# Kernel tuning notes

Measured on AMD Instinct MI355X. Metric: run time of the kernel, lower is better.

Reference implementation:

```python
import jax, jax.numpy as jnp
import numpy as np

DIM = 768
H = 12          # num query heads
KV = 6          # num kv heads
GS = H // KV    # group size = 2
HD = DIM // H   # head dim = 64


def setup_inputs() -> dict:
    key = jax.random.key(0)
    ks = jax.random.split(key, 6)
    B, P = 8, 1024
    s = DIM ** -0.5
    x = jax.random.normal(ks[0], (B, P, DIM), dtype=jnp.float32)
    Wq = jax.random.normal(ks[1], (DIM, DIM), dtype=jnp.float32) * s
    Wk = jax.random.normal(ks[2], (DIM, KV * HD), dtype=jnp.float32) * s
    Wv = jax.random.normal(ks[3], (DIM, KV * HD), dtype=jnp.float32) * s
    Wp = jax.random.normal(ks[4], (DIM, DIM), dtype=jnp.float32) * s
    bp = jnp.zeros((DIM,), dtype=jnp.float32)
    return {"x": x, "Wq": Wq, "Wk": Wk, "Wv": Wv, "Wp": Wp, "bp": bp}


def reference(x, Wq, Wk, Wv, Wp, bp):
    B, P, C = x.shape
    scale = HD ** -0.5
    # projections; consecutive heads i*GS..(i+1)*GS-1 form kv-group i (torch.split dim=1)
    q = (x @ Wq).reshape(B, P, KV, GS, HD).transpose(0, 2, 3, 1, 4) * scale  # [B,KV,GS,P,d]
    k = (x @ Wk).reshape(B, P, KV, HD).transpose(0, 2, 1, 3)                 # [B,KV,P,d]
    v = (x @ Wv).reshape(B, P, KV, HD).transpose(0, 2, 1, 3)                 # [B,KV,P,d]

    scores = jnp.einsum('bghqd,bgkd->bghqk', q, k)      # [B,KV,GS,P,P]
    w = jax.nn.softmax(scores, axis=-1)                  # attn_drop=0 (eval)
    att = jnp.einsum('bghqk,bgkd->bghqd', w, v)          # [B,KV,GS,P,d]

    # per-group row-matched gaussian-ish noise (torch get_gaussian), vectorized over KV groups
    y = P * HD
    flat = att.reshape(B, KV, GS, y)                     # rows = groups within kv-group
    M = jax.random.uniform(jax.random.key(42), (KV, GS, y), dtype=flat.dtype)
    di = jnp.arange(min(GS, y))
    M = M.at[:, di, di].set(0.0)                         # sparse: zero diagonal
    m_mean = M.mean(axis=-1, keepdims=True)
    m_std = jnp.std(M, axis=-1, ddof=1, keepdims=True)   # torch.std is unbiased
    m_std = jnp.where(m_std == 0, jnp.ones_like(m_std), m_std)
    Z = (M - m_mean) / m_std                             # [KV,GS,y], shared across batch
    r_mean = flat.mean(axis=-1, keepdims=True)           # [B,KV,GS,1]
    r_std = jnp.std(flat, axis=-1, ddof=1, keepdims=True)
    flat = flat - (Z[None] * r_std + r_mean)

    att = flat.reshape(B, KV, GS, P, HD).reshape(B, H, P, HD)
    out = att.transpose(0, 2, 1, 3).reshape(B, P, C) @ Wp + bp  # proj_drop=0
    return out
```

## Files before the change

kernel.cpp:

```cpp
#include <hip/hip_runtime.h>
#include <hip/hip_bf16.h>
#include <math.h>


#define NTHREADS 256

typedef __bf16 bf16x8 __attribute__((ext_vector_type(8)));
typedef float f32x4 __attribute__((ext_vector_type(4)));

#define MFMA16(a, b, c) __builtin_amdgcn_mfma_f32_16x16x32_bf16(a, b, c, 0, 0, 0)

#define QSCALE 0.18033688011112042f

__device__ __forceinline__ float fexp2(float x) {
#if __has_builtin(__builtin_amdgcn_exp2f)
    return __builtin_amdgcn_exp2f(x);
#else
    return __expf(x * 0.6931471805599453f);
#endif
}

__device__ __forceinline__ void gload16(const void* g, void* l) {
    __builtin_amdgcn_global_load_lds(
        (const __attribute__((address_space(1))) void*)g,
        (__attribute__((address_space(3))) void*)l, 16, 0, 0);
}

__device__ __forceinline__ unsigned rotl_u32(unsigned x, int r) {
    return (x << r) | (x >> (32 - r));
}
__device__ __forceinline__ void threefry_0_42(unsigned x0, unsigned x1,
                                              unsigned& o0, unsigned& o1) {
    const unsigned ks0 = 0u, ks1 = 42u, ks2 = 0u ^ 42u ^ 0x1BD11BDAu;
    x0 += ks0; x1 += ks1;
#define R4(a,b,c,d) \
    x0 += x1; x1 = rotl_u32(x1,a); x1 ^= x0; \
    x0 += x1; x1 = rotl_u32(x1,b); x1 ^= x0; \
    x0 += x1; x1 = rotl_u32(x1,c); x1 ^= x0; \
    x0 += x1; x1 = rotl_u32(x1,d); x1 ^= x0;
    R4(13,15,26,6)   x0 += ks1; x1 += ks2 + 1u;
    R4(17,29,16,24)  x0 += ks2; x1 += ks0 + 2u;
    R4(13,15,26,6)   x0 += ks0; x1 += ks1 + 3u;
    R4(17,29,16,24)  x0 += ks1; x1 += ks2 + 4u;
    R4(13,15,26,6)   x0 += ks2; x1 += ks0 + 5u;
#undef R4
    o0 = x0; o1 = x1;
}
__device__ __forceinline__ float tf_uniform(unsigned i) {
    unsigned o0, o1;
    threefry_0_42(0u, i, o0, o1);
    unsigned bits = o0 ^ o1;
    return __uint_as_float((bits >> 9) | 0x3f800000u) - 1.0f;
}

__device__ __forceinline__ float wave_sum64(float v) {
#pragma unroll
    for (int off = 32; off; off >>= 1) v += __shfl_xor(v, off, 64);
    return v;
}

__device__ __forceinline__ unsigned short bf16_rne(float x) {
    unsigned u = __float_as_uint(x);
    return (unsigned short)((u + 0x7fffu + ((u >> 16) & 1u)) >> 16);
}
__device__ __forceinline__ unsigned pack_bf16x2(float lo, float hi) {
    return (unsigned)bf16_rne(lo) | ((unsigned)bf16_rne(hi) << 16);
}
__device__ __forceinline__ float bfu(unsigned v) {
    return __uint_as_float(v << 16);
}

__global__ __launch_bounds__(NTHREADS) void prep_k(
    const float* __restrict__ x, const float* __restrict__ Wq,
    const float* __restrict__ Wk, const float* __restrict__ Wv,
    const float* __restrict__ Wp,
    unsigned short* __restrict__ xb, unsigned short* __restrict__ wqt,
    unsigned short* __restrict__ wkt, unsigned short* __restrict__ wvt,
    unsigned short* __restrict__ wpt,
    unsigned short* __restrict__ zb, float* __restrict__ zpart)
{
    __shared__ float rbuf[8];
    int blk = blockIdx.x;
    if (blk < 1536) {
#pragma unroll
        for (int j = 0; j < 4; ++j) {
            int i = blk * 1024 + j * 256 + threadIdx.x;
            float4 v = ((const float4*)x)[i];
            uint2 u;
            u.x = pack_bf16x2(v.x, v.y);
            u.y = pack_bf16x2(v.z, v.w);
            *(uint2*)(xb + (size_t)i * 4) = u;
        }
    } else if (blk < 1920) {
        int zc = blk - 1536;
        int row = zc >> 5, chunk = zc & 31;
        int g = row & 1;
        int j0 = chunk * 2048;
        float sum = 0.f, sumsq = 0.f;
        for (int t = threadIdx.x; t < 2048; t += NTHREADS) {
            int j = j0 + t;
            unsigned i = (unsigned)row * 65536u + (unsigned)j;
            float m = tf_uniform(i);
            if (j == g) m = 0.f;
            zb[i] = bf16_rne(m);
            sum += m; sumsq += m * m;
        }
        sum = wave_sum64(sum); sumsq = wave_sum64(sumsq);
        int lane = threadIdx.x & 63, wv = threadIdx.x >> 6;
        if (lane == 0) { rbuf[wv] = sum; rbuf[4 + wv] = sumsq; }
        __syncthreads();
        if (threadIdx.x == 0) {
            zpart[zc * 2]     = rbuf[0] + rbuf[1] + rbuf[2] + rbuf[3];
            zpart[zc * 2 + 1] = rbuf[4] + rbuf[5] + rbuf[6] + rbuf[7];
        }
    } else {
        int id = blk - 1920;
        const float* W; unsigned short* Wt; int N;
        if (id < 144)      { W = Wq; Wt = wqt; N = 768; }
        else if (id < 216) { W = Wk; Wt = wkt; N = 384; id -= 144; }
        else if (id < 288) { W = Wv; Wt = wvt; N = 384; id -= 216; }
        else               { W = Wp; Wt = wpt; N = 768; id -= 288; }
        int ntn = N >> 6;
        int kt = id / ntn, nt = id % ntn;
        int k0 = kt * 64, n0 = nt * 64;
        int t = threadIdx.x;
        int tn = t & 63, tk = t >> 6;
        float r[16];
#pragma unroll
        for (int j = 0; j < 16; ++j)
            r[j] = W[(size_t)(k0 + tk * 16 + j) * N + n0 + tn];
        uint4 u0, u1;
        u0.x = pack_bf16x2(r[0], r[1]);   u0.y = pack_bf16x2(r[2], r[3]);
        u0.z = pack_bf16x2(r[4], r[5]);   u0.w = pack_bf16x2(r[6], r[7]);
        u1.x = pack_bf16x2(r[8], r[9]);   u1.y = pack_bf16x2(r[10], r[11]);
        u1.z = pack_bf16x2(r[12], r[13]); u1.w = pack_bf16x2(r[14], r[15]);
        unsigned short* dst = Wt + (size_t)(n0 + tn) * 768 + k0 + tk * 16;
        *(uint4*)dst = u0;
        *(uint4*)(dst + 8) = u1;
    }
}

__device__ __forceinline__ void mfma_tile_compute(
    const unsigned short* __restrict__ A, const unsigned short* __restrict__ Bt,
    int row0, int col0,
    unsigned short* As0, unsigned short* Bs0,
    unsigned short* As1, unsigned short* Bs1,
    f32x4 acc[4][4])
{
    const int tid = threadIdx.x;
    const int w = tid >> 6, lane = tid & 63;
    const int c = lane & 15, g = lane >> 4;
    const int m0 = (w & 1) * 64, n0 = (w >> 1) * 64;

#pragma unroll
    for (int mi = 0; mi < 4; ++mi)
#pragma unroll
        for (int ni = 0; ni < 4; ++ni) acc[mi][ni] = (f32x4){0.f, 0.f, 0.f, 0.f};

    const unsigned short* Ag0 = A + (size_t)(row0 + w * 16 + c) * 768 + g * 8;
    const unsigned short* Ag1 = A + (size_t)(row0 + (w + 4) * 16 + c) * 768 + g * 8;
    const unsigned short* Bg0 = Bt + (size_t)(col0 + w * 16 + c) * 768 + g * 8;
    const unsigned short* Bg1 = Bt + (size_t)(col0 + (w + 4) * 16 + c) * 768 + g * 8;
    const int l0 = w * 1024 + lane * 8;
    const int l1 = (w + 4) * 1024 + lane * 8;

#define STAGE_TILE(k0, As, Bs) do {                                           \
        gload16(Ag0 + (k0),      (As) + l0);                                  \
        gload16(Ag0 + (k0) + 32, (As) + l0 + 512);                            \
        gload16(Ag1 + (k0),      (As) + l1);                                  \
        gload16(Ag1 + (k0) + 32, (As) + l1 + 512);                            \
        gload16(Bg0 + (k0),      (Bs) + l0);                                  \
        gload16(Bg0 + (k0) + 32, (Bs) + l0 + 512);                            \
        gload16(Bg1 + (k0),      (Bs) + l1);                                  \
        gload16(Bg1 + (k0) + 32, (Bs) + l1 + 512);                            \
    } while (0)

#define COMPUTE_TILE(As, Bs) do {                                             \
        _Pragma("unroll")                                                     \
        for (int ks = 0; ks < 2; ++ks) {                                      \
            bf16x8 aA[4], bB[4];                                              \
            _Pragma("unroll")                                                 \
            for (int mi = 0; mi < 4; ++mi)                                    \
                aA[mi] = *(const bf16x8*)&(As)[(size_t)((m0 >> 4) + mi) * 1024\
                                               + ks * 512 + g * 128 + c * 8]; \
            _Pragma("unroll")                                                 \
            for (int ni = 0; ni < 4; ++ni)                                    \
                bB[ni] = *(const bf16x8*)&(Bs)[(size_t)((n0 >> 4) + ni) * 1024\
                                               + ks * 512 + g * 128 + c * 8]; \
            _Pragma("unroll")                                                 \
            for (int mi = 0; mi < 4; ++mi)                                    \
                _Pragma("unroll")                                             \
                for (int ni = 0; ni < 4; ++ni)                                \
                    acc[mi][ni] = MFMA16(aA[mi], bB[ni], acc[mi][ni]);        \
        }                                                                     \
    } while (0)

    STAGE_TILE(0, As0, Bs0);
    __syncthreads();
    for (int k0 = 64; k0 <= 576; k0 += 128) {
        STAGE_TILE(k0, As1, Bs1);
        COMPUTE_TILE(As0, Bs0);
        __syncthreads();
        STAGE_TILE(k0 + 64, As0, Bs0);
        COMPUTE_TILE(As1, Bs1);
        __syncthreads();
    }
    STAGE_TILE(704, As1, Bs1);
    COMPUTE_TILE(As0, Bs0);
    __syncthreads();
    COMPUTE_TILE(As1, Bs1);

#undef STAGE_TILE
#undef COMPUTE_TILE
}

__global__ __launch_bounds__(NTHREADS) void qkv_mfma_k(
    const unsigned short* __restrict__ xb, const unsigned short* __restrict__ wqt,
    const unsigned short* __restrict__ wkt, const unsigned short* __restrict__ wvt,
    unsigned short* __restrict__ qbh, unsigned short* __restrict__ kb2,
    unsigned short* __restrict__ vb2)
{
    __shared__ unsigned short As0[8192], Bs0[8192], As1[8192], Bs1[8192];
    int nb = blockIdx.x;
    int y0 = blockIdx.y * 128;
    f32x4 acc[4][4];

    const int tid = threadIdx.x;
    const int w = tid >> 6, lane = tid & 63;
    const int c = lane & 15, g = lane >> 4;
    const int m0 = (w & 1) * 64, n0 = (w >> 1) * 64;

    if (nb < 9) {
        int row0 = (nb < 6) ? nb * 128 : (nb - 6) * 128;
        const unsigned short* Wt = (nb < 6) ? wqt : wkt;
        mfma_tile_compute(Wt, xb, row0, y0, As0, Bs0, As1, Bs1, acc);
        float scale = (nb < 6) ? QSCALE : 1.0f;
#pragma unroll
        for (int mi = 0; mi < 4; ++mi) {
            int ocol = row0 + m0 + mi * 16 + g * 4;
#pragma unroll
            for (int ni = 0; ni < 4; ++ni) {
                int pglob = y0 + n0 + ni * 16 + c;
                int b = pglob >> 10, pin = pglob & 1023;
                ushort4 u;
                u.x = bf16_rne(acc[mi][ni][0] * scale);
                u.y = bf16_rne(acc[mi][ni][1] * scale);
                u.z = bf16_rne(acc[mi][ni][2] * scale);
                u.w = bf16_rne(acc[mi][ni][3] * scale);
                if (nb < 6) {
                    int h = ocol >> 6, d0 = ocol & 63;
                    *(ushort4*)&qbh[(((size_t)b * 12 + h) * 1024 + pin) * 64 + d0] = u;
                } else {
                    int kv = ocol >> 6, d0 = ocol & 63;
                    int kt = pin >> 7, key = pin & 127;
                    *(ushort4*)&kb2[((((size_t)(b * 6 + kv) * 8 + kt) * 8 + (d0 >> 3)) * 128
                                     + key) * 8 + (d0 & 7)] = u;
                }
            }
        }
    } else {
        int col0 = (nb - 9) * 128;
        mfma_tile_compute(xb, wvt, y0, col0, As0, Bs0, As1, Bs1, acc);
#pragma unroll
        for (int mi = 0; mi < 4; ++mi) {
            int pglob = y0 + m0 + mi * 16 + g * 4;
            int b = pglob >> 10, pin = pglob & 1023;
            int kt = pin >> 7, pg = (pin & 127) >> 3, p8 = pin & 7;
#pragma unroll
            for (int ni = 0; ni < 4; ++ni) {
                int vcol = col0 + n0 + ni * 16 + c;
                int kv = vcol >> 6, d = vcol & 63;
                ushort4 u;
                u.x = bf16_rne(acc[mi][ni][0]);
                u.y = bf16_rne(acc[mi][ni][1]);
                u.z = bf16_rne(acc[mi][ni][2]);
                u.w = bf16_rne(acc[mi][ni][3]);
                *(ushort4*)&vb2[((((size_t)(b * 6 + kv) * 8 + kt) * 16 + pg) * 64 + d) * 8 + p8] = u;
            }
        }
    }
}

__global__ __launch_bounds__(NTHREADS) void proj_mfma_k(
    const unsigned short* __restrict__ attb, const unsigned short* __restrict__ wpt,
    const float* __restrict__ bp, float* __restrict__ out)
{
    __shared__ unsigned short As0[8192], Bs0[8192], As1[8192], Bs1[8192];
    int row0 = blockIdx.x * 128, col0 = blockIdx.y * 128;
    f32x4 acc[4][4];
    mfma_tile_compute(wpt, attb, row0, col0, As0, Bs0, As1, Bs1, acc);

    const int tid = threadIdx.x;
    const int w = tid >> 6, lane = tid & 63;
    const int c = lane & 15, g = lane >> 4;
    const int m0 = (w & 1) * 64, n0 = (w >> 1) * 64;
#pragma unroll
    for (int mi = 0; mi < 4; ++mi) {
        int ocol = row0 + m0 + mi * 16 + g * 4;
        float4 bias = *(const float4*)&bp[ocol];
#pragma unroll
        for (int ni = 0; ni < 4; ++ni) {
            int p = col0 + n0 + ni * 16 + c;
            float4 u;
            u.x = acc[mi][ni][0] + bias.x;
            u.y = acc[mi][ni][1] + bias.y;
            u.z = acc[mi][ni][2] + bias.z;
            u.w = acc[mi][ni][3] + bias.w;
            *(float4*)&out[(size_t)p * 768 + ocol] = u;
        }
    }
}

#define LDP 136
__global__ __launch_bounds__(NTHREADS) void attn_mfma_k(
    const unsigned short* __restrict__ qbh, const unsigned short* __restrict__ kb2,
    const unsigned short* __restrict__ vb2, unsigned short* __restrict__ attb,
    float* __restrict__ spart)
{
    __shared__ unsigned short P_lds[4 * 32 * LDP];
    __shared__ float l_s[4][32];
    __shared__ float sbuf[8];

    const int qt0 = blockIdx.x * 128;
    const int h = blockIdx.y, b = blockIdx.z, kv = h >> 1;
    const int tid = threadIdx.x;
    const int w = tid >> 6, lane = tid & 63;
    const int c = lane & 15, g = lane >> 4;

    const unsigned short* qh = qbh + (((size_t)b * 12 + h) * 1024 + qt0 + w * 32) * 64;
    const unsigned short* kbase = kb2 + ((size_t)(b * 6 + kv) * 8) * 8192;
    const unsigned short* vbase = vb2 + ((size_t)(b * 6 + kv) * 8) * 8192;
    unsigned short* Pw = P_lds + w * 32 * LDP;

    bf16x8 bQ[2][2];
#pragma unroll
    for (int ks = 0; ks < 2; ++ks) {
        bQ[ks][0] = *(const bf16x8*)(qh + (size_t)(c) * 64 + ks * 32 + g * 8);
        bQ[ks][1] = *(const bf16x8*)(qh + (size_t)(16 + c) * 64 + ks * 32 + g * 8);
    }

    f32x4 O[2][4];
#pragma unroll
    for (int i = 0; i < 2; ++i)
#pragma unroll
        for (int j = 0; j < 4; ++j) O[i][j] = (f32x4){0.f, 0.f, 0.f, 0.f};
    float l_r[2] = {0.f, 0.f};

    for (int t = 0; t < 8; ++t) {
        const unsigned short* kt = kbase + (size_t)t * 8192;
        const unsigned short* vt = vbase + (size_t)t * 8192;

        bf16x8 aK[2][8];
#pragma unroll
        for (int ks = 0; ks < 2; ++ks)
#pragma unroll
            for (int mb = 0; mb < 8; ++mb)
                aK[ks][mb] = *(const bf16x8*)(kt + ((size_t)(ks * 4 + g) * 128 + mb * 16 + c) * 8);

        f32x4 S[8][2];
#pragma unroll
        for (int mb = 0; mb < 8; ++mb) {
            S[mb][0] = (f32x4){0.f, 0.f, 0.f, 0.f};
            S[mb][1] = (f32x4){0.f, 0.f, 0.f, 0.f};
        }
#pragma unroll
        for (int ks = 0; ks < 2; ++ks)
#pragma unroll
            for (int mb = 0; mb < 8; ++mb) {
                S[mb][0] = MFMA16(aK[ks][mb], bQ[ks][0], S[mb][0]);
                S[mb][1] = MFMA16(aK[ks][mb], bQ[ks][1], S[mb][1]);
            }

        bf16x8 bV[4][4];
#pragma unroll
        for (int ks = 0; ks < 4; ++ks)
#pragma unroll
            for (int nb = 0; nb < 4; ++nb)
                bV[ks][nb] = *(const bf16x8*)(vt + ((size_t)(ks * 4 + g) * 64 + nb * 16 + c) * 8);

#pragma unroll
        for (int qn = 0; qn < 2; ++qn) {
            float lt = 0.f;
#pragma unroll
            for (int mb = 0; mb < 8; ++mb) {
                float p0 = fexp2(S[mb][qn][0]);
                float p1 = fexp2(S[mb][qn][1]);
                float p2 = fexp2(S[mb][qn][2]);
                float p3 = fexp2(S[mb][qn][3]);
                lt += (p0 + p1) + (p2 + p3);
                uint2 uu;
                uu.x = pack_bf16x2(p0, p1);
                uu.y = pack_bf16x2(p2, p3);
                *(uint2*)&Pw[(size_t)(qn * 16 + c) * LDP + mb * 16 + g * 4] = uu;
            }
            lt += __shfl_xor(lt, 16, 64);
            lt += __shfl_xor(lt, 32, 64);
            l_r[qn] += lt;
        }

#pragma unroll
        for (int ks = 0; ks < 4; ++ks) {
            bf16x8 aP0 = *(const bf16x8*)&Pw[(size_t)(c) * LDP + ks * 32 + g * 8];
            bf16x8 aP1 = *(const bf16x8*)&Pw[(size_t)(16 + c) * LDP + ks * 32 + g * 8];
#pragma unroll
            for (int nb = 0; nb < 4; ++nb) {
                O[0][nb] = MFMA16(aP0, bV[ks][nb], O[0][nb]);
                O[1][nb] = MFMA16(aP1, bV[ks][nb], O[1][nb]);
            }
        }
    }
    if (g == 0) { l_s[w][c] = l_r[0]; l_s[w][16 + c] = l_r[1]; }
    f32x4 li0 = *(f32x4*)&l_s[w][g * 4];
    f32x4 li1 = *(f32x4*)&l_s[w][16 + g * 4];
    float inv0[4], inv1[4];
#pragma unroll
    for (int r = 0; r < 4; ++r) { inv0[r] = 1.f / li0[r]; inv1[r] = 1.f / li1[r]; }
    unsigned short* ob = attb + ((size_t)b * 1024 + qt0 + w * 32) * 768 + h * 64;
    float psum = 0.f, psumsq = 0.f;
#pragma unroll
    for (int r = 0; r < 4; ++r) {
#pragma unroll
        for (int nb = 0; nb < 4; ++nb) {
            float o0 = O[0][nb][r] * inv0[r];
            float o1 = O[1][nb][r] * inv1[r];
            psum += o0 + o1;
            psumsq += o0 * o0 + o1 * o1;
            ob[(size_t)(g * 4 + r) * 768 + nb * 16 + c]      = bf16_rne(o0);
            ob[(size_t)(16 + g * 4 + r) * 768 + nb * 16 + c] = bf16_rne(o1);
        }
    }
    psum = wave_sum64(psum); psumsq = wave_sum64(psumsq);
    if (lane == 0) { sbuf[w] = psum; sbuf[4 + w] = psumsq; }
    __syncthreads();
    if (tid == 0) {
        int idx = ((b * 12 + h) * 8 + blockIdx.x) * 2;
        spart[idx]     = sbuf[0] + sbuf[1] + sbuf[2] + sbuf[3];
        spart[idx + 1] = sbuf[4] + sbuf[5] + sbuf[6] + sbuf[7];
    }
}

__global__ __launch_bounds__(NTHREADS) void stats2_k(
    unsigned short* __restrict__ attb, const unsigned short* __restrict__ zb,
    const float* __restrict__ spart, const float* __restrict__ zpart)
{
    int blk = blockIdx.x;
    int bh = blk >> 3, ch = blk & 7;
    int b = bh / 12, h = bh % 12;
    float zs = 0.f, zs2 = 0.f, rs = 0.f, rs2 = 0.f;
#pragma unroll
    for (int cc = 0; cc < 32; ++cc) {
        zs  += zpart[(h * 32 + cc) * 2];
        zs2 += zpart[(h * 32 + cc) * 2 + 1];
    }
#pragma unroll
    for (int cc = 0; cc < 8; ++cc) {
        rs  += spart[(bh * 8 + cc) * 2];
        rs2 += spart[(bh * 8 + cc) * 2 + 1];
    }
    float m_mean = zs * (1.f / 65536.f);
    float m_var  = (zs2 - 65536.f * m_mean * m_mean) * (1.f / 65535.f);
    float m_sd   = sqrtf(fmaxf(m_var, 0.f));
    if (m_sd == 0.f) m_sd = 1.f;
    float r_mean = rs * (1.f / 65536.f);
    float r_var  = (rs2 - 65536.f * r_mean * r_mean) * (1.f / 65535.f);
    float r_sd   = sqrtf(fmaxf(r_var, 0.f));
    float a = r_sd / m_sd;
    float bc = m_mean * a - r_mean;

    unsigned short* base = attb + ((size_t)b * 1024 + ch * 128) * 768 + h * 64;
    const unsigned short* zrow = zb + (size_t)h * 65536 + (size_t)ch * 8192;
    for (int f = threadIdx.x; f < 1024; f += NTHREADS) {
        int p = f >> 3, dq = (f & 7) * 8;
        unsigned short* ptr = base + (size_t)p * 768 + dq;
        uint4 u = *(const uint4*)ptr;
        uint4 zu = *(const uint4*)(zrow + (size_t)f * 8);
        float v0 = bfu(u.x)       - bfu(zu.x)       * a + bc;
        float v1 = bfu(u.x >> 16) - bfu(zu.x >> 16) * a + bc;
        float v2 = bfu(u.y)       - bfu(zu.y)       * a + bc;
        float v3 = bfu(u.y >> 16) - bfu(zu.y >> 16) * a + bc;
        float v4 = bfu(u.z)       - bfu(zu.z)       * a + bc;
        float v5 = bfu(u.z >> 16) - bfu(zu.z >> 16) * a + bc;
        float v6 = bfu(u.w)       - bfu(zu.w)       * a + bc;
        float v7 = bfu(u.w >> 16) - bfu(zu.w >> 16) * a + bc;
        uint4 o;
        o.x = pack_bf16x2(v0, v1);
        o.y = pack_bf16x2(v2, v3);
        o.z = pack_bf16x2(v4, v5);
        o.w = pack_bf16x2(v6, v7);
        *(uint4*)ptr = o;
    }
}

extern "C" void kernel_launch(void* const* d_in, const int* in_sizes, int n_in,
                              void* d_out, int out_size, void* d_ws, size_t ws_size,
                              hipStream_t stream) {
    const float* x  = (const float*)d_in[0];
    const float* Wq = (const float*)d_in[1];
    const float* Wk = (const float*)d_in[2];
    const float* Wv = (const float*)d_in[3];
    const float* Wp = (const float*)d_in[4];
    const float* bp = (const float*)d_in[5];
    float* out = (float*)d_out;

    float* ws    = (float*)d_ws;
    float* zpart = ws;
    float* spart = zpart + 768;
    unsigned short* zb   = (unsigned short*)(spart + 1536);
    unsigned short* xb   = zb + 786432;
    unsigned short* wqt  = xb + 6291456;
    unsigned short* wkt  = wqt + 589824;
    unsigned short* wvt  = wkt + 294912;
    unsigned short* wpt  = wvt + 294912;
    unsigned short* qbh  = wpt + 589824;
    unsigned short* kb2  = qbh + 6291456;
    unsigned short* vb2  = kb2 + 3145728;
    unsigned short* attb = vb2 + 3145728;

    prep_k<<<2352, NTHREADS, 0, stream>>>(x, Wq, Wk, Wv, Wp,
                                          xb, wqt, wkt, wvt, wpt, zb, zpart);
    qkv_mfma_k<<<dim3(12, 64), NTHREADS, 0, stream>>>(xb, wqt, wkt, wvt, qbh, kb2, vb2);
    attn_mfma_k<<<dim3(8, 12, 8), NTHREADS, 0, stream>>>(qbh, kb2, vb2, attb, spart);
    stats2_k<<<768, NTHREADS, 0, stream>>>(attb, zb, spart, zpart);
    proj_mfma_k<<<dim3(6, 64), NTHREADS, 0, stream>>>(attb, wpt, bp, out);
}
```

Measured before the change: 224.3 us.

## Deepen GEMM prefetch with vmcnt waits and remap blocks for XCD locality

The shared GEMM loop now issues two tile loads up front and uses explicit s_waitcnt vmcnt plus raw barriers, so one tile's global-to-LDS load overlaps the other tile's MFMA compute instead of waiting on full __syncthreads. The QKV, attention and projection kernels also switch to 1D grids with a swizzled block-to-tile mapping, so blocks that share a kv-group or weight panel land on the same XCD and reuse its L2. The hand-written vmcnt counts depend on exactly how many loads STAGE_TILE issues, and a wrong count would race.

```diff
diff --git a/kernel.cpp b/kernel.cpp
--- a/kernel.cpp
+++ b/kernel.cpp
@@ -195,23 +195,33 @@
         }                                                                     \
     } while (0)
 
-    STAGE_TILE(0, As0, Bs0);
-    __syncthreads();
-    for (int k0 = 64; k0 <= 576; k0 += 128) {
-        STAGE_TILE(k0, As1, Bs1);
+#define WAITV8  asm volatile("s_waitcnt vmcnt(8)" ::: "memory")
+#define WAITV0  asm volatile("s_waitcnt vmcnt(0)" ::: "memory")
+#define BAR     __builtin_amdgcn_s_barrier()
+
+    STAGE_TILE(0,  As0, Bs0);
+    STAGE_TILE(64, As1, Bs1);
+#pragma unroll 1
+    for (int t = 0; t < 10; t += 2) {
+        WAITV8; BAR;
         COMPUTE_TILE(As0, Bs0);
-        __syncthreads();
-        STAGE_TILE(k0 + 64, As0, Bs0);
+        BAR;
+        STAGE_TILE((t + 2) * 64, As0, Bs0);
+        WAITV8; BAR;
         COMPUTE_TILE(As1, Bs1);
-        __syncthreads();
-    }
-    STAGE_TILE(704, As1, Bs1);
+        BAR;
+        STAGE_TILE((t + 3) * 64, As1, Bs1);
+    }
+    WAITV8; BAR;
     COMPUTE_TILE(As0, Bs0);
-    __syncthreads();
+    WAITV0; BAR;
     COMPUTE_TILE(As1, Bs1);
 
 #undef STAGE_TILE
 #undef COMPUTE_TILE
+#undef WAITV8
+#undef WAITV0
+#undef BAR
 }
 
 __global__ __launch_bounds__(NTHREADS) void qkv_mfma_k(
@@ -221,8 +231,11 @@
     unsigned short* __restrict__ vb2)
 {
     __shared__ unsigned short As0[8192], Bs0[8192], As1[8192], Bs1[8192];
-    int nb = blockIdx.x;
-    int y0 = blockIdx.y * 128;
+    int id = blockIdx.x;
+    int xcd = id & 7, slot = id >> 3;
+    int y0i = xcd + ((slot & 7) << 3);
+    int nb  = slot >> 3;
+    int y0 = y0i * 128;
     f32x4 acc[4][4];
 
     const int tid = threadIdx.x;
@@ -286,7 +299,11 @@
     const float* __restrict__ bp, float* __restrict__ out)
 {
     __shared__ unsigned short As0[8192], Bs0[8192], As1[8192], Bs1[8192];
-    int row0 = blockIdx.x * 128, col0 = blockIdx.y * 128;
+    int id = blockIdx.x;
+    int xcd = id & 7, slot = id >> 3;
+    int col0i = xcd + ((slot & 7) << 3);
+    int row0i = slot >> 3;
+    int row0 = row0i * 128, col0 = col0i * 128;
     f32x4 acc[4][4];
     mfma_tile_compute(wpt, attb, row0, col0, As0, Bs0, As1, Bs1, acc);
 
@@ -321,8 +338,15 @@
     __shared__ float l_s[4][32];
     __shared__ float sbuf[8];
 
-    const int qt0 = blockIdx.x * 128;
-    const int h = blockIdx.y, b = blockIdx.z, kv = h >> 1;
+    int id = blockIdx.x;
+    int xcd = id & 7, slot = id >> 3;
+    int grp = slot % 6, member = slot / 6;
+    int g48 = xcd + 8 * grp;
+    int b = g48 / 6, kv = g48 % 6;
+    int h = kv * 2 + (member & 1);
+    int qtile = member >> 1;
+    const int qt0 = qtile * 128;
+
     const int tid = threadIdx.x;
     const int w = tid >> 6, lane = tid & 63;
     const int c = lane & 15, g = lane >> 4;
@@ -433,7 +457,7 @@
     if (lane == 0) { sbuf[w] = psum; sbuf[4 + w] = psumsq; }
     __syncthreads();
     if (tid == 0) {
-        int idx = ((b * 12 + h) * 8 + blockIdx.x) * 2;
+        int idx = ((b * 12 + h) * 8 + qtile) * 2;
         spart[idx]     = sbuf[0] + sbuf[1] + sbuf[2] + sbuf[3];
         spart[idx + 1] = sbuf[4] + sbuf[5] + sbuf[6] + sbuf[7];
     }
@@ -518,8 +542,8 @@
 
     prep_k<<<2352, NTHREADS, 0, stream>>>(x, Wq, Wk, Wv, Wp,
                                           xb, wqt, wkt, wvt, wpt, zb, zpart);
-    qkv_mfma_k<<<dim3(12, 64), NTHREADS, 0, stream>>>(xb, wqt, wkt, wvt, qbh, kb2, vb2);
-    attn_mfma_k<<<dim3(8, 12, 8), NTHREADS, 0, stream>>>(qbh, kb2, vb2, attb, spart);
+    qkv_mfma_k<<<768, NTHREADS, 0, stream>>>(xb, wqt, wkt, wvt, qbh, kb2, vb2);
+    attn_mfma_k<<<768, NTHREADS, 0, stream>>>(qbh, kb2, vb2, attb, spart);
     stats2_k<<<768, NTHREADS, 0, stream>>>(attb, zb, spart, zpart);
-    proj_mfma_k<<<dim3(6, 64), NTHREADS, 0, stream>>>(attb, wpt, bp, out);
-}
+    proj_mfma_k<<<384, NTHREADS, 0, stream>>>(attb, wpt, bp, out);
+}
```

Result: faster. 215.9 us (-3.7%).
